# Optimization experiments

Hardware: AMD Instinct MI355X
Metric: run time of the kernel (lower is better)

## Reference

```python
import jax, jax.numpy as jnp
import numpy as np

D_IN, D_HID, N_TOK = 2048, 8192, 8192

def _ternary(key, shape):
    # ternary {-1, 0, 1} weights stored as float32
    return jax.random.randint(key, shape, -1, 2).astype(jnp.float32)

def setup_inputs() -> dict:
    key = jax.random.key(0)
    kx, k1, k2, kh, k3 = jax.random.split(key, 5)
    return {
        "x": jax.random.normal(kx, (N_TOK, D_IN), dtype=jnp.float32),
        "W1": _ternary(k1, (D_HID, D_IN)),   # gate proj
        "W2": _ternary(k2, (D_HID, D_IN)),   # value proj
        "Wh": _ternary(kh, (D_HID, D_HID)),  # hidden layer (depth-1 == 1)
        "W3": _ternary(k3, (D_IN, D_HID)),   # output proj
        # per-layer dequant scales (scalar), ~1/sqrt(fan_in)
        "s1": jnp.float32(1.0 / np.sqrt(D_IN)),
        "s2": jnp.float32(1.0 / np.sqrt(D_IN)),
        "sh": jnp.float32(1.0 / np.sqrt(D_HID)),
        "s3": jnp.float32(1.0 / np.sqrt(D_HID)),
    }

def _tlin(x, W, s):
    # ternary packed linear: dequantized matmul, no bias
    return jnp.einsum('td,hd->th', x, W) * s

def reference(x, W1, W2, Wh, W3, s1, s2, sh, s3):
    h = jax.nn.silu(_tlin(x, W1, s1)) * _tlin(x, W2, s2)   # SwiGLU entry
    h = jax.nn.gelu(_tlin(h, Wh, sh), approximate=False)    # hidden block (depth-1)
    return _tlin(h, W3, s3)                                 # [N_TOK, D_IN]
```

## Files before the change

### kernel.cpp

```cpp
#include <hip/hip_runtime.h>
#include <hip/hip_bf16.h>
#include <stdint.h>

typedef __bf16 bf16;
typedef __bf16 bf16x8 __attribute__((ext_vector_type(8)));
typedef float f32x4 __attribute__((ext_vector_type(4)));

typedef uint32_t __attribute__((address_space(1))) * gptr_as1;
typedef uint32_t __attribute__((address_space(3))) * lptr_as3;

__device__ __forceinline__ void async16(const void* g, void* l) {
    __builtin_amdgcn_global_load_lds((gptr_as1)(uintptr_t)g,
                                     (lptr_as3)(uintptr_t)l,
                                     16, 0, 0);
}

__device__ __forceinline__ void bar() {
    asm volatile("" ::: "memory");
    __builtin_amdgcn_s_barrier();
    asm volatile("" ::: "memory");
}

__global__ void cvt_f32_bf16_kernel(const float* __restrict__ src,
                                    bf16* __restrict__ dst, int n8) {
    int i = blockIdx.x * blockDim.x + threadIdx.x;
    if (i >= n8) return;
    const float4* s = reinterpret_cast<const float4*>(src);
    float4 a = s[2 * (size_t)i], b = s[2 * (size_t)i + 1];
    bf16x8 v;
    v[0] = (bf16)a.x; v[1] = (bf16)a.y; v[2] = (bf16)a.z; v[3] = (bf16)a.w;
    v[4] = (bf16)b.x; v[5] = (bf16)b.y; v[6] = (bf16)b.z; v[7] = (bf16)b.w;
    *reinterpret_cast<bf16x8*>(dst + (size_t)i * 8) = v;
}

__global__ void cvt_ilv_kernel(const float* __restrict__ src,
                               bf16* __restrict__ dst, int n8, int sel) {
    int i = blockIdx.x * blockDim.x + threadIdx.x;
    if (i >= n8) return;
    const int row = i >> 8;
    const int c = i & 255;
    const int drow = ((row >> 4) << 5) + (sel << 4) + (row & 15);
    const float4* s = reinterpret_cast<const float4*>(src);
    float4 a = s[2 * (size_t)i], b = s[2 * (size_t)i + 1];
    bf16x8 v;
    v[0] = (bf16)a.x; v[1] = (bf16)a.y; v[2] = (bf16)a.z; v[3] = (bf16)a.w;
    v[4] = (bf16)b.x; v[5] = (bf16)b.y; v[6] = (bf16)b.z; v[7] = (bf16)b.w;
    *reinterpret_cast<bf16x8*>(dst + ((size_t)drow * 256 + c) * 8) = v;
}

template <int EPI, int K>
__global__ __launch_bounds__(512, 4)
void gemm2b(const bf16* __restrict__ A, const bf16* __restrict__ B,
            void* __restrict__ Cout, const float* __restrict__ s1p,
            const float* __restrict__ s2p, int N, int ldh) {
    __shared__ __align__(16) char sm[49152];

    const int tid = threadIdx.x;
    const int w = tid >> 6, l = tid & 63;
    const int wr = w >> 1, wc = w & 1;

    const int gx = gridDim.x;
    const int nwg = gx * (int)gridDim.y;
    const int orig = blockIdx.y * gx + blockIdx.x;
    const int wg = (orig & 7) * (nwg >> 3) + (orig >> 3);
    const int bm = wg / gx, bn = wg % gx;

    constexpr int NT = K / 64;

    f32x4 acc[4][4] = {};

    char* const bufA = sm;
    char* const bufB = sm + 32768;
    const int arow = bm * 256, brow = bn * 128;

    const int srow_in = l >> 3;
    const int scolb = ((l & 7) ^ srow_in) << 4;
    auto STAGE = [&](char* ldsT, const bf16* g, int grow0, int kt, int r0) {
        const int rr = r0 + w * 8 + srow_in;
        const char* gp = (const char*)(g + (size_t)(grow0 + rr) * K + kt * 64) + scolb;
        async16(gp, ldsT + r0 * 128 + w * 1024);
    };

    const int rlane = l & 15;
    const int chi = (l >> 4) << 4;
    auto FRAG = [&](const char* tb, int row, int ks) -> bf16x8 {
        const int cb = (ks * 64 + chi) ^ ((row & 7) << 4);
        return *reinterpret_cast<const bf16x8*>(tb + row * 128 + cb);
    };

#pragma unroll 1
    for (int kt = 0; kt < NT; ++kt) {
        STAGE(bufA, A, arow, kt, 0);   STAGE(bufA, A, arow, kt, 64);
        STAGE(bufA, A, arow, kt, 128); STAGE(bufA, A, arow, kt, 192);
        STAGE(bufB, B, brow, kt, 0);   STAGE(bufB, B, brow, kt, 64);
        asm volatile("s_waitcnt vmcnt(0)" ::: "memory");
        bar();
#pragma unroll
        for (int ks = 0; ks < 2; ++ks) {
            bf16x8 av[4], bv[4];
#pragma unroll
            for (int i = 0; i < 4; ++i)
                av[i] = FRAG(bufA, wr * 64 + i * 16 + rlane, ks);
#pragma unroll
            for (int j = 0; j < 4; ++j)
                bv[j] = FRAG(bufB, wc * 64 + j * 16 + rlane, ks);
            __builtin_amdgcn_s_setprio(1);
#pragma unroll
            for (int i = 0; i < 4; ++i)
#pragma unroll
                for (int j = 0; j < 4; ++j)
                    acc[i][j] = __builtin_amdgcn_mfma_f32_16x16x32_bf16(av[i], bv[j], acc[i][j], 0, 0, 0);
            __builtin_amdgcn_s_setprio(0);
        }
        bar();
    }

    const float s1 = s1p[0];
    const int r0 = bm * 256 + wr * 64 + ((l >> 4) << 2);
    if constexpr (EPI == 2) {
        const float s2 = s2p[0];
        const int hcb = (bn * 4 + wc * 2) * 16 + rlane;
#pragma unroll
        for (int i = 0; i < 4; ++i)
#pragma unroll
            for (int jp = 0; jp < 2; ++jp)
#pragma unroll
                for (int q = 0; q < 4; ++q) {
                    float g = acc[i][2 * jp][q] * s1;
                    float v = acc[i][2 * jp + 1][q] * s2;
                    float sig = 1.0f / (1.0f + __expf(-g));
                    ((bf16*)Cout)[(size_t)(r0 + i * 16 + q) * ldh + hcb + jp * 16] =
                        (bf16)(g * sig * v);
                }
    } else {
        const int c0 = bn * 128 + wc * 64 + rlane;
#pragma unroll
        for (int i = 0; i < 4; ++i)
#pragma unroll
            for (int j = 0; j < 4; ++j)
#pragma unroll
                for (int q = 0; q < 4; ++q) {
                    float v = acc[i][j][q] * s1;
                    size_t idx = (size_t)(r0 + i * 16 + q) * N + (c0 + j * 16);
                    if constexpr (EPI == 0) {
                        float g = 0.5f * v * (1.0f + erff(v * 0.70710678118654752f));
                        ((bf16*)Cout)[idx] = (bf16)g;
                    } else {
                        ((float*)Cout)[idx] = v;
                    }
                }
    }
}

extern "C" void kernel_launch(void* const* d_in, const int* in_sizes, int n_in,
                              void* d_out, int out_size, void* d_ws, size_t ws_size,
                              hipStream_t stream) {
    constexpr int NTOK = 8192, DIN = 2048, DHID = 8192;

    const float* x  = (const float*)d_in[0];
    const float* W1 = (const float*)d_in[1];
    const float* W2 = (const float*)d_in[2];
    const float* Wh = (const float*)d_in[3];
    const float* W3 = (const float*)d_in[4];
    const float* s1 = (const float*)d_in[5];
    const float* s2 = (const float*)d_in[6];
    const float* sh = (const float*)d_in[7];
    const float* s3 = (const float*)d_in[8];
    float* out = (float*)d_out;

    char* ws = (char*)d_ws;
    size_t off = 0;
    bf16* xb   = (bf16*)(ws + off); off += (size_t)NTOK * DIN * 2;
    bf16* w12b = (bf16*)(ws + off); off += (size_t)2 * DHID * DIN * 2;
    bf16* w3b  = (bf16*)(ws + off); off += (size_t)DIN * DHID * 2;
    bf16* whb  = (bf16*)(ws + off); off += (size_t)DHID * DHID * 2;
    bf16* h1   = (bf16*)(ws + off); off += (size_t)NTOK * DHID * 2;
    bf16* h2   = (bf16*)(ws + off); off += (size_t)NTOK * DHID * 2;
    if (ws_size < off) return;

    auto cvt = [&](const float* s, bf16* d, size_t n) {
        int n8 = (int)(n / 8);
        cvt_f32_bf16_kernel<<<(n8 + 255) / 256, 256, 0, stream>>>(s, d, n8);
    };
    cvt(x,  xb,  (size_t)NTOK * DIN);
    cvt(Wh, whb, (size_t)DHID * DHID);
    cvt(W3, w3b, (size_t)DIN * DHID);
    {
        int n8 = (int)((size_t)DHID * DIN / 8);
        cvt_ilv_kernel<<<(n8 + 255) / 256, 256, 0, stream>>>(W1, w12b, n8, 0);
        cvt_ilv_kernel<<<(n8 + 255) / 256, 256, 0, stream>>>(W2, w12b, n8, 1);
    }

    gemm2b<2, DIN><<<dim3(2 * DHID / 128, NTOK / 256), 512, 0, stream>>>(
        xb, w12b, h1, s1, s2, 2 * DHID, DHID);
    gemm2b<0, DHID><<<dim3(DHID / 128, NTOK / 256), 512, 0, stream>>>(
        h1, whb, h2, sh, sh, DHID, DHID);
    gemm2b<1, DHID><<<dim3(DIN / 128, NTOK / 256), 512, 0, stream>>>(
        h2, w3b, out, s3, s3, DIN, DIN);
}
```

Measured before the change: 1.852 ms.

## Double-buffer LDS tiles and shrink block tile to 256x64 with 32-row waves

Moves the GEMM from a single-buffered 256x128 tile to a 256x64 tile with two LDS buffers, prefetching tile kt+2 while tile kt is computed. Each wave now owns a 32x64 slice with all B rows shared, and the grid doubles along N. The aim is to hide global-load latency behind MFMA work. In exchange, arithmetic intensity per tile drops, LDS use rises to 80KB (which may cut occupancy), and the wait/barrier ordering has to be exactly right.

```diff
diff --git a/kernel.cpp b/kernel.cpp
--- a/kernel.cpp
+++ b/kernel.cpp
@@ -50,14 +50,13 @@
 
 template <int EPI, int K>
 __global__ __launch_bounds__(512, 4)
-void gemm2b(const bf16* __restrict__ A, const bf16* __restrict__ B,
-            void* __restrict__ Cout, const float* __restrict__ s1p,
-            const float* __restrict__ s2p, int N, int ldh) {
-    __shared__ __align__(16) char sm[49152];
+void gemmtlp(const bf16* __restrict__ A, const bf16* __restrict__ B,
+             void* __restrict__ Cout, const float* __restrict__ s1p,
+             const float* __restrict__ s2p, int N, int ldh) {
+    __shared__ __align__(16) char sm[81920];
 
     const int tid = threadIdx.x;
     const int w = tid >> 6, l = tid & 63;
-    const int wr = w >> 1, wc = w & 1;
 
     const int gx = gridDim.x;
     const int nwg = gx * (int)gridDim.y;
@@ -67,11 +66,9 @@
 
     constexpr int NT = K / 64;
 
-    f32x4 acc[4][4] = {};
-
-    char* const bufA = sm;
-    char* const bufB = sm + 32768;
-    const int arow = bm * 256, brow = bn * 128;
+    f32x4 acc[2][4] = {};
+
+    const int arow = bm * 256, brow = bn * 64;
 
     const int srow_in = l >> 3;
     const int scolb = ((l & 7) ^ srow_in) << 4;
@@ -80,6 +77,12 @@
         const char* gp = (const char*)(g + (size_t)(grow0 + rr) * K + kt * 64) + scolb;
         async16(gp, ldsT + r0 * 128 + w * 1024);
     };
+    auto STAGE_TILE = [&](int kt) {
+        char* base = sm + (kt & 1) * 40960;
+        STAGE(base, A, arow, kt, 0);   STAGE(base, A, arow, kt, 64);
+        STAGE(base, A, arow, kt, 128); STAGE(base, A, arow, kt, 192);
+        STAGE(base + 32768, B, brow, kt, 0);
+    };
 
     const int rlane = l & 15;
     const int chi = (l >> 4) << 4;
@@ -88,40 +91,47 @@
         return *reinterpret_cast<const bf16x8*>(tb + row * 128 + cb);
     };
 
+    STAGE_TILE(0);
+    STAGE_TILE(1);
+    asm volatile("s_waitcnt vmcnt(5)" ::: "memory");
+    bar();
+
 #pragma unroll 1
     for (int kt = 0; kt < NT; ++kt) {
-        STAGE(bufA, A, arow, kt, 0);   STAGE(bufA, A, arow, kt, 64);
-        STAGE(bufA, A, arow, kt, 128); STAGE(bufA, A, arow, kt, 192);
-        STAGE(bufB, B, brow, kt, 0);   STAGE(bufB, B, brow, kt, 64);
+        const char* bA = sm + (kt & 1) * 40960;
+        const char* bB = bA + 32768;
+
+        bf16x8 av[2][2], bv[4][2];
+#pragma unroll
+        for (int ks = 0; ks < 2; ++ks) {
+#pragma unroll
+            for (int i = 0; i < 2; ++i)
+                av[i][ks] = FRAG(bA, w * 32 + i * 16 + rlane, ks);
+#pragma unroll
+            for (int j = 0; j < 4; ++j)
+                bv[j][ks] = FRAG(bB, j * 16 + rlane, ks);
+        }
+        __builtin_amdgcn_s_setprio(1);
+#pragma unroll
+        for (int ks = 0; ks < 2; ++ks)
+#pragma unroll
+            for (int i = 0; i < 2; ++i)
+#pragma unroll
+                for (int j = 0; j < 4; ++j)
+                    acc[i][j] = __builtin_amdgcn_mfma_f32_16x16x32_bf16(av[i][ks], bv[j][ks], acc[i][j], 0, 0, 0);
+        __builtin_amdgcn_s_setprio(0);
         asm volatile("s_waitcnt vmcnt(0)" ::: "memory");
         bar();
-#pragma unroll
-        for (int ks = 0; ks < 2; ++ks) {
-            bf16x8 av[4], bv[4];
-#pragma unroll
-            for (int i = 0; i < 4; ++i)
-                av[i] = FRAG(bufA, wr * 64 + i * 16 + rlane, ks);
-#pragma unroll
-            for (int j = 0; j < 4; ++j)
-                bv[j] = FRAG(bufB, wc * 64 + j * 16 + rlane, ks);
-            __builtin_amdgcn_s_setprio(1);
-#pragma unroll
-            for (int i = 0; i < 4; ++i)
-#pragma unroll
-                for (int j = 0; j < 4; ++j)
-                    acc[i][j] = __builtin_amdgcn_mfma_f32_16x16x32_bf16(av[i], bv[j], acc[i][j], 0, 0, 0);
-            __builtin_amdgcn_s_setprio(0);
-        }
-        bar();
+        if (kt + 2 < NT) STAGE_TILE(kt + 2);
     }
 
     const float s1 = s1p[0];
-    const int r0 = bm * 256 + wr * 64 + ((l >> 4) << 2);
+    const int r0 = bm * 256 + w * 32 + ((l >> 4) << 2);
     if constexpr (EPI == 2) {
         const float s2 = s2p[0];
-        const int hcb = (bn * 4 + wc * 2) * 16 + rlane;
-#pragma unroll
-        for (int i = 0; i < 4; ++i)
+        const int hcb = bn * 32 + rlane;
+#pragma unroll
+        for (int i = 0; i < 2; ++i)
 #pragma unroll
             for (int jp = 0; jp < 2; ++jp)
 #pragma unroll
@@ -133,9 +143,9 @@
                         (bf16)(g * sig * v);
                 }
     } else {
-        const int c0 = bn * 128 + wc * 64 + rlane;
-#pragma unroll
-        for (int i = 0; i < 4; ++i)
+        const int c0 = bn * 64 + rlane;
+#pragma unroll
+        for (int i = 0; i < 2; ++i)
 #pragma unroll
             for (int j = 0; j < 4; ++j)
 #pragma unroll
@@ -191,10 +201,10 @@
         cvt_ilv_kernel<<<(n8 + 255) / 256, 256, 0, stream>>>(W2, w12b, n8, 1);
     }
 
-    gemm2b<2, DIN><<<dim3(2 * DHID / 128, NTOK / 256), 512, 0, stream>>>(
+    gemmtlp<2, DIN><<<dim3(2 * DHID / 64, NTOK / 256), 512, 0, stream>>>(
         xb, w12b, h1, s1, s2, 2 * DHID, DHID);
-    gemm2b<0, DHID><<<dim3(DHID / 128, NTOK / 256), 512, 0, stream>>>(
+    gemmtlp<0, DHID><<<dim3(DHID / 64, NTOK / 256), 512, 0, stream>>>(
         h1, whb, h2, sh, sh, DHID, DHID);
-    gemm2b<1, DHID><<<dim3(DIN / 128, NTOK / 256), 512, 0, stream>>>(
+    gemmtlp<1, DHID><<<dim3(DIN / 64, NTOK / 256), 512, 0, stream>>>(
         h2, w3b, out, s3, s3, DIN, DIN);
 }
```

After: 2.101 ms. 13.5% more time.

## Enlarge GEMM tiles to 256x256 with double-buffered LDS prefetch

Applied to the files above, without the earlier changes.

Replaces the 256x128 tile, 8-wave GEMM with a 256x256 tile computed by 4 waves. Each wave now owns a 128x128 sub-tile with an 8x8 grid of MFMA accumulators. LDS grows to 128KB and holds two buffers, so the next K-tile is loaded asynchronously while the current one is computed, which removes the stall on every K step. This raises arithmetic intensity and cuts global/LDS traffic per FLOP. In exchange it needs very high register use and runs one 4-wave block per CU, which weakens latency hiding and leaves fewer blocks to balance across CUs for the narrow output GEMM.

```diff
diff --git a/kernel.cpp b/kernel.cpp
--- a/kernel.cpp
+++ b/kernel.cpp
@@ -49,11 +49,11 @@
 }
 
 template <int EPI, int K>
-__global__ __launch_bounds__(512, 4)
-void gemm2b(const bf16* __restrict__ A, const bf16* __restrict__ B,
-            void* __restrict__ Cout, const float* __restrict__ s1p,
-            const float* __restrict__ s2p, int N, int ldh) {
-    __shared__ __align__(16) char sm[49152];
+__global__ __launch_bounds__(256, 1)
+void gemmfat(const bf16* __restrict__ A, const bf16* __restrict__ B,
+             void* __restrict__ Cout, const float* __restrict__ s1p,
+             const float* __restrict__ s2p, int N, int ldh) {
+    __shared__ __align__(16) char sm[131072];
 
     const int tid = threadIdx.x;
     const int w = tid >> 6, l = tid & 63;
@@ -67,11 +67,9 @@
 
     constexpr int NT = K / 64;
 
-    f32x4 acc[4][4] = {};
-
-    char* const bufA = sm;
-    char* const bufB = sm + 32768;
-    const int arow = bm * 256, brow = bn * 128;
+    f32x4 acc[8][8] = {};
+
+    const int arow = bm * 256, brow = bn * 256;
 
     const int srow_in = l >> 3;
     const int scolb = ((l & 7) ^ srow_in) << 4;
@@ -80,6 +78,13 @@
         const char* gp = (const char*)(g + (size_t)(grow0 + rr) * K + kt * 64) + scolb;
         async16(gp, ldsT + r0 * 128 + w * 1024);
     };
+    auto STAGE_TILE = [&](int kt) {
+        char* base = sm + (kt & 1) * 65536;
+#pragma unroll
+        for (int r = 0; r < 8; ++r) STAGE(base, A, arow, kt, r * 32);
+#pragma unroll
+        for (int r = 0; r < 8; ++r) STAGE(base + 32768, B, brow, kt, r * 32);
+    };
 
     const int rlane = l & 15;
     const int chi = (l >> 4) << 4;
@@ -88,42 +93,61 @@
         return *reinterpret_cast<const bf16x8*>(tb + row * 128 + cb);
     };
 
+    STAGE_TILE(0);
+    asm volatile("s_waitcnt vmcnt(0)" ::: "memory");
+    bar();
+
 #pragma unroll 1
     for (int kt = 0; kt < NT; ++kt) {
-        STAGE(bufA, A, arow, kt, 0);   STAGE(bufA, A, arow, kt, 64);
-        STAGE(bufA, A, arow, kt, 128); STAGE(bufA, A, arow, kt, 192);
-        STAGE(bufB, B, brow, kt, 0);   STAGE(bufB, B, brow, kt, 64);
+        const char* bA = sm + (kt & 1) * 65536;
+        const char* bB = bA + 32768;
+        if (kt + 1 < NT) STAGE_TILE(kt + 1);
+
+        bf16x8 av[8], bv[8];
+#pragma unroll
+        for (int i = 0; i < 8; ++i)
+            av[i] = FRAG(bA, wr * 128 + i * 16 + rlane, 0);
+#pragma unroll
+        for (int j = 0; j < 8; ++j)
+            bv[j] = FRAG(bB, wc * 128 + j * 16 + rlane, 0);
+        asm volatile("s_waitcnt lgkmcnt(0)" ::: "memory");
+        __builtin_amdgcn_sched_barrier(0);
+        __builtin_amdgcn_s_setprio(1);
+#pragma unroll
+        for (int i = 0; i < 8; ++i)
+#pragma unroll
+            for (int j = 0; j < 8; ++j)
+                acc[i][j] = __builtin_amdgcn_mfma_f32_16x16x32_bf16(av[i], bv[j], acc[i][j], 0, 0, 0);
+        __builtin_amdgcn_s_setprio(0);
+        bf16x8 av1[8], bv1[8];
+#pragma unroll
+        for (int i = 0; i < 8; ++i)
+            av1[i] = FRAG(bA, wr * 128 + i * 16 + rlane, 1);
+#pragma unroll
+        for (int j = 0; j < 8; ++j)
+            bv1[j] = FRAG(bB, wc * 128 + j * 16 + rlane, 1);
+        asm volatile("s_waitcnt lgkmcnt(0)" ::: "memory");
+        __builtin_amdgcn_sched_barrier(0);
+        __builtin_amdgcn_s_setprio(1);
+#pragma unroll
+        for (int i = 0; i < 8; ++i)
+#pragma unroll
+            for (int j = 0; j < 8; ++j)
+                acc[i][j] = __builtin_amdgcn_mfma_f32_16x16x32_bf16(av1[i], bv1[j], acc[i][j], 0, 0, 0);
+        __builtin_amdgcn_s_setprio(0);
         asm volatile("s_waitcnt vmcnt(0)" ::: "memory");
         bar();
-#pragma unroll
-        for (int ks = 0; ks < 2; ++ks) {
-            bf16x8 av[4], bv[4];
-#pragma unroll
-            for (int i = 0; i < 4; ++i)
-                av[i] = FRAG(bufA, wr * 64 + i * 16 + rlane, ks);
-#pragma unroll
-            for (int j = 0; j < 4; ++j)
-                bv[j] = FRAG(bufB, wc * 64 + j * 16 + rlane, ks);
-            __builtin_amdgcn_s_setprio(1);
-#pragma unroll
-            for (int i = 0; i < 4; ++i)
-#pragma unroll
-                for (int j = 0; j < 4; ++j)
-                    acc[i][j] = __builtin_amdgcn_mfma_f32_16x16x32_bf16(av[i], bv[j], acc[i][j], 0, 0, 0);
-            __builtin_amdgcn_s_setprio(0);
-        }
-        bar();
     }
 
     const float s1 = s1p[0];
-    const int r0 = bm * 256 + wr * 64 + ((l >> 4) << 2);
+    const int r0 = bm * 256 + wr * 128 + ((l >> 4) << 2);
     if constexpr (EPI == 2) {
         const float s2 = s2p[0];
-        const int hcb = (bn * 4 + wc * 2) * 16 + rlane;
-#pragma unroll
-        for (int i = 0; i < 4; ++i)
-#pragma unroll
-            for (int jp = 0; jp < 2; ++jp)
+        const int hcb = (bn * 8 + wc * 4) * 16 + rlane;
+#pragma unroll
+        for (int i = 0; i < 8; ++i)
+#pragma unroll
+            for (int jp = 0; jp < 4; ++jp)
 #pragma unroll
                 for (int q = 0; q < 4; ++q) {
                     float g = acc[i][2 * jp][q] * s1;
@@ -133,11 +157,11 @@
                         (bf16)(g * sig * v);
                 }
     } else {
-        const int c0 = bn * 128 + wc * 64 + rlane;
-#pragma unroll
-        for (int i = 0; i < 4; ++i)
-#pragma unroll
-            for (int j = 0; j < 4; ++j)
+        const int c0 = bn * 256 + wc * 128 + rlane;
+#pragma unroll
+        for (int i = 0; i < 8; ++i)
+#pragma unroll
+            for (int j = 0; j < 8; ++j)
 #pragma unroll
                 for (int q = 0; q < 4; ++q) {
                     float v = acc[i][j][q] * s1;
@@ -191,10 +215,10 @@
         cvt_ilv_kernel<<<(n8 + 255) / 256, 256, 0, stream>>>(W2, w12b, n8, 1);
     }
 
-    gemm2b<2, DIN><<<dim3(2 * DHID / 128, NTOK / 256), 512, 0, stream>>>(
+    gemmfat<2, DIN><<<dim3(2 * DHID / 256, NTOK / 256), 256, 0, stream>>>(
         xb, w12b, h1, s1, s2, 2 * DHID, DHID);
-    gemm2b<0, DHID><<<dim3(DHID / 128, NTOK / 256), 512, 0, stream>>>(
+    gemmfat<0, DHID><<<dim3(DHID / 256, NTOK / 256), 256, 0, stream>>>(
         h1, whb, h2, sh, sh, DHID, DHID);
-    gemm2b<1, DHID><<<dim3(DIN / 128, NTOK / 256), 512, 0, stream>>>(
+    gemmfat<1, DHID><<<dim3(DIN / 256, NTOK / 256), 256, 0, stream>>>(
         h2, w3b, out, s3, s3, DIN, DIN);
 }
```

After: 7.028 ms. +279.6%, slower.

## Use 256x256 tiles with a four-stage async LDS pipeline in the GEMM

Applied to the files above, without the earlier changes.

Replaces the single-buffered 256x128 GEMM with a 256x256 tile, a K-step of 32 and a four-slot LDS ring. Three tiles are prefetched ahead, with vmcnt-based waits and one barrier per step, so global loads overlap the MFMA work instead of draining before every step. Each wave now holds an 8x4 accumulator block, which raises arithmetic intensity per LDS read. The cost is 128 KB of LDS and a larger register footprint, which allows only one workgroup per CU.

```diff
diff --git a/kernel.cpp b/kernel.cpp
--- a/kernel.cpp
+++ b/kernel.cpp
@@ -49,15 +49,15 @@
 }
 
 template <int EPI, int K>
-__global__ __launch_bounds__(512, 4)
-void gemm2b(const bf16* __restrict__ A, const bf16* __restrict__ B,
+__global__ __launch_bounds__(512, 1)
+void gemm4s(const bf16* __restrict__ A, const bf16* __restrict__ B,
             void* __restrict__ Cout, const float* __restrict__ s1p,
             const float* __restrict__ s2p, int N, int ldh) {
-    __shared__ __align__(16) char sm[49152];
+    __shared__ __align__(16) char sm[131072];
 
     const int tid = threadIdx.x;
     const int w = tid >> 6, l = tid & 63;
-    const int wr = w >> 1, wc = w & 1;
+    const int wr = w >> 2, wc = w & 3;
 
     const int gx = gridDim.x;
     const int nwg = gx * (int)gridDim.y;
@@ -65,63 +65,84 @@
     const int wg = (orig & 7) * (nwg >> 3) + (orig >> 3);
     const int bm = wg / gx, bn = wg % gx;
 
-    constexpr int NT = K / 64;
-
-    f32x4 acc[4][4] = {};
-
-    char* const bufA = sm;
-    char* const bufB = sm + 32768;
-    const int arow = bm * 256, brow = bn * 128;
-
-    const int srow_in = l >> 3;
-    const int scolb = ((l & 7) ^ srow_in) << 4;
-    auto STAGE = [&](char* ldsT, const bf16* g, int grow0, int kt, int r0) {
-        const int rr = r0 + w * 8 + srow_in;
-        const char* gp = (const char*)(g + (size_t)(grow0 + rr) * K + kt * 64) + scolb;
-        async16(gp, ldsT + r0 * 128 + w * 1024);
+    constexpr int NT = K / 32;
+
+    f32x4 acc[8][4] = {};
+
+    const int arow = bm * 256, brow = bn * 256;
+
+    const int sr = l >> 2;
+    const int sg = ((l & 3) ^ ((l >> 3) & 3)) << 4;
+    const char* qa0 = (const char*)(A + (size_t)(arow +   0 + w * 16 + sr) * K) + sg;
+    const char* qa1 = (const char*)(A + (size_t)(arow + 128 + w * 16 + sr) * K) + sg;
+    const char* qb0 = (const char*)(B + (size_t)(brow +   0 + w * 16 + sr) * K) + sg;
+    const char* qb1 = (const char*)(B + (size_t)(brow + 128 + w * 16 + sr) * K) + sg;
+    const int ldw = w * 1024;
+    auto STAGE_TILE = [&](char* slot) {
+        async16(qa0, slot +     0 + ldw);
+        async16(qa1, slot +  8192 + ldw);
+        async16(qb0, slot + 16384 + ldw);
+        async16(qb1, slot + 24576 + ldw);
+        qa0 += 64; qa1 += 64; qb0 += 64; qb1 += 64;
     };
 
     const int rlane = l & 15;
     const int chi = (l >> 4) << 4;
-    auto FRAG = [&](const char* tb, int row, int ks) -> bf16x8 {
-        const int cb = (ks * 64 + chi) ^ ((row & 7) << 4);
-        return *reinterpret_cast<const bf16x8*>(tb + row * 128 + cb);
+    const int swz = ((rlane >> 1) & 3) << 4;
+    const int offA = (wr * 128 + rlane) * 64 + (chi ^ swz);
+    const int offB = (wc * 64 + rlane) * 64 + (chi ^ swz);
+    const char* const pA0 = sm +      0 + offA;
+    const char* const pA1 = sm +  32768 + offA;
+    const char* const pA2 = sm +  65536 + offA;
+    const char* const pA3 = sm +  98304 + offA;
+    const char* const pB0 = sm +  16384 + offB;
+    const char* const pB1 = sm +  49152 + offB;
+    const char* const pB2 = sm +  81920 + offB;
+    const char* const pB3 = sm + 114688 + offB;
+
+    STAGE_TILE(sm);
+    STAGE_TILE(sm + 32768);
+    STAGE_TILE(sm + 65536);
+    asm volatile("s_waitcnt vmcnt(8)" ::: "memory");
+    bar();
+
+    auto body = [&](int kt, const char* pa, const char* pb, char* nslot) {
+        if (kt + 3 < NT) STAGE_TILE(nslot);
+        bf16x8 bv[4], av[8];
+#pragma unroll
+        for (int j = 0; j < 4; ++j)
+            bv[j] = *reinterpret_cast<const bf16x8*>(pb + j * 1024);
+#pragma unroll
+        for (int i = 0; i < 8; ++i)
+            av[i] = *reinterpret_cast<const bf16x8*>(pa + i * 1024);
+        __builtin_amdgcn_s_setprio(1);
+#pragma unroll
+        for (int i = 0; i < 8; ++i)
+#pragma unroll
+            for (int j = 0; j < 4; ++j)
+                acc[i][j] = __builtin_amdgcn_mfma_f32_16x16x32_bf16(av[i], bv[j], acc[i][j], 0, 0, 0);
+        __builtin_amdgcn_s_setprio(0);
+        if (kt + 3 < NT)      { asm volatile("s_waitcnt vmcnt(8)" ::: "memory"); }
+        else if (kt == NT - 3) { asm volatile("s_waitcnt vmcnt(4)" ::: "memory"); }
+        else if (kt == NT - 2) { asm volatile("s_waitcnt vmcnt(0)" ::: "memory"); }
+        bar();
     };
 
 #pragma unroll 1
-    for (int kt = 0; kt < NT; ++kt) {
-        STAGE(bufA, A, arow, kt, 0);   STAGE(bufA, A, arow, kt, 64);
-        STAGE(bufA, A, arow, kt, 128); STAGE(bufA, A, arow, kt, 192);
-        STAGE(bufB, B, brow, kt, 0);   STAGE(bufB, B, brow, kt, 64);
-        asm volatile("s_waitcnt vmcnt(0)" ::: "memory");
-        bar();
-#pragma unroll
-        for (int ks = 0; ks < 2; ++ks) {
-            bf16x8 av[4], bv[4];
-#pragma unroll
-            for (int i = 0; i < 4; ++i)
-                av[i] = FRAG(bufA, wr * 64 + i * 16 + rlane, ks);
-#pragma unroll
-            for (int j = 0; j < 4; ++j)
-                bv[j] = FRAG(bufB, wc * 64 + j * 16 + rlane, ks);
-            __builtin_amdgcn_s_setprio(1);
-#pragma unroll
-            for (int i = 0; i < 4; ++i)
-#pragma unroll
-                for (int j = 0; j < 4; ++j)
-                    acc[i][j] = __builtin_amdgcn_mfma_f32_16x16x32_bf16(av[i], bv[j], acc[i][j], 0, 0, 0);
-            __builtin_amdgcn_s_setprio(0);
-        }
-        bar();
+    for (int kt = 0; kt < NT; kt += 4) {
+        body(kt + 0, pA0, pB0, sm + 98304);
+        body(kt + 1, pA1, pB1, sm);
+        body(kt + 2, pA2, pB2, sm + 32768);
+        body(kt + 3, pA3, pB3, sm + 65536);
     }
 
     const float s1 = s1p[0];
-    const int r0 = bm * 256 + wr * 64 + ((l >> 4) << 2);
+    const int r0 = bm * 256 + wr * 128 + ((l >> 4) << 2);
     if constexpr (EPI == 2) {
         const float s2 = s2p[0];
-        const int hcb = (bn * 4 + wc * 2) * 16 + rlane;
-#pragma unroll
-        for (int i = 0; i < 4; ++i)
+        const int hcb = (bn * 8 + wc * 2) * 16 + rlane;
+#pragma unroll
+        for (int i = 0; i < 8; ++i)
 #pragma unroll
             for (int jp = 0; jp < 2; ++jp)
 #pragma unroll
@@ -133,9 +154,9 @@
                         (bf16)(g * sig * v);
                 }
     } else {
-        const int c0 = bn * 128 + wc * 64 + rlane;
-#pragma unroll
-        for (int i = 0; i < 4; ++i)
+        const int c0 = bn * 256 + wc * 64 + rlane;
+#pragma unroll
+        for (int i = 0; i < 8; ++i)
 #pragma unroll
             for (int j = 0; j < 4; ++j)
 #pragma unroll
@@ -191,10 +212,10 @@
         cvt_ilv_kernel<<<(n8 + 255) / 256, 256, 0, stream>>>(W2, w12b, n8, 1);
     }
 
-    gemm2b<2, DIN><<<dim3(2 * DHID / 128, NTOK / 256), 512, 0, stream>>>(
+    gemm4s<2, DIN><<<dim3(2 * DHID / 256, NTOK / 256), 512, 0, stream>>>(
         xb, w12b, h1, s1, s2, 2 * DHID, DHID);
-    gemm2b<0, DHID><<<dim3(DHID / 128, NTOK / 256), 512, 0, stream>>>(
+    gemm4s<0, DHID><<<dim3(DHID / 256, NTOK / 256), 512, 0, stream>>>(
         h1, whb, h2, sh, sh, DHID, DHID);
-    gemm2b<1, DHID><<<dim3(DIN / 128, NTOK / 256), 512, 0, stream>>>(
+    gemm4s<1, DHID><<<dim3(DIN / 256, NTOK / 256), 512, 0, stream>>>(
         h2, w3b, out, s3, s3, DIN, DIN);
 }
```

Measured after the change: 2.061 ms. +11.3%, slower.
